# Kernel optimization log

Measured on AMD Instinct MI355X. Metric: run time of the kernel, lower is better.

Reference implementation:

```python
import jax, jax.numpy as jnp
import numpy as np

_IDENTITY = jnp.array([1, 0, 0, 0], dtype=jnp.float32)

G, T, P, B = 512, 128, 256, 512  # num_graphs, max_terms, n_params, batch


def setup_inputs() -> dict:
    key = jax.random.key(0)
    k0, k1, k2, k3, k4 = jax.random.split(key, 5)
    psi_const = jax.random.randint(k0, (G, T), 0, 2).astype(jnp.int32)
    psi_params = jax.random.randint(k1, (G, T, P), 0, 2).astype(jnp.float32)
    phi_const = jax.random.randint(k2, (G, T), 0, 2).astype(jnp.int32)
    phi_params = jax.random.randint(k3, (G, T, P), 0, 2).astype(jnp.float32)
    param_vals = jax.random.randint(k4, (B, P), 0, 2).astype(jnp.float32)
    return {
        "psi_const": psi_const,
        "psi_params": psi_params,
        "phi_const": phi_const,
        "phi_params": phi_params,
        "param_vals": param_vals,
    }


def reference(psi_const, psi_params, phi_const, phi_params, param_vals):
    # GF(2) matmul: contract bitmasks with binary parameter values, mod 2.
    # psi_params: (G,T,P), param_vals: (B,P) -> (B,G,T)
    psi = jnp.mod(psi_const[None].astype(jnp.float32)
                  + jnp.einsum("gtp,bp->bgt", psi_params, param_vals), 2.0)
    phi = jnp.mod(phi_const[None].astype(jnp.float32)
                  + jnp.einsum("gtp,bp->bgt", phi_params, param_vals), 2.0)
    # Elementwise parity product and mod-2 sum over terms -> (B,G)
    exponent = jnp.mod(psi * phi, 2.0)
    sum_exponents = jnp.mod(jnp.sum(exponent, axis=-1), 2.0)
    # Parity-to-sign: (-1)^e = 1 - 2e, embedded as exact scalar (B,G,4)
    summands_exact = (1.0 - 2.0 * sum_exponents)[..., None] * _IDENTITY
    return summands_exact
```

## Files before the change

### kernel.cpp

```cpp
#include <hip/hip_runtime.h>

typedef unsigned long long u64;

#define G 512
#define T 128
#define P 256
#define B 512

struct __align__(16) U64x2 { u64 x, y; };

__global__ __launch_bounds__(256) void pack_pv_kernel(
    const float* __restrict__ pv, u64* __restrict__ out)
{
    int lane = threadIdx.x & 63;
    int wave = threadIdx.x >> 6;
    int row  = blockIdx.x * 4 + wave;
    const float4* src = (const float4*)(pv + (size_t)row * P);
    float4 f = src[lane];
    u64 w0 = __ballot(f.x != 0.0f);
    u64 w1 = __ballot(f.y != 0.0f);
    u64 w2 = __ballot(f.z != 0.0f);
    u64 w3 = __ballot(f.w != 0.0f);
    if (lane == 0) {
        out[row * 4 + 0] = w0;
        out[row * 4 + 1] = w1;
        out[row * 4 + 2] = w2;
        out[row * 4 + 3] = w3;
    }
}

__global__ __launch_bounds__(512) void pi_main_kernel(
    const int*   __restrict__ psi_const,
    const float* __restrict__ psi_params,
    const int*   __restrict__ phi_const,
    const float* __restrict__ phi_params,
    const u64*   __restrict__ pv,
    float4*      __restrict__ out)
{
    __shared__ __align__(16) u64 rows[T * 8];
    __shared__ unsigned code_sm[T];

    const int g    = blockIdx.x;
    const int tid  = threadIdx.x;
    const int lane = tid & 63;
    const int wave = tid >> 6;

    if (tid < T) {
        unsigned pc = ((unsigned)psi_const[g * T + tid]) & 1u;
        unsigned qc = ((unsigned)phi_const[g * T + tid]) & 1u;
        code_sm[tid] = pc | (qc << 1);
    }

    for (int i = 0; i < 32; ++i) {
        int r = wave * 32 + i;
        int t = r & (T - 1);
        const float* mat = (r < T) ? psi_params : phi_params;
        int off = (r < T) ? 0 : 4;
        const float4* src = (const float4*)(mat + ((size_t)g * T + t) * P);
        float4 f = src[lane];
        u64 w0 = __ballot(f.x != 0.0f);
        u64 w1 = __ballot(f.y != 0.0f);
        u64 w2 = __ballot(f.z != 0.0f);
        u64 w3 = __ballot(f.w != 0.0f);
        if (lane == 0) {
            U64x2* d = (U64x2*)&rows[t * 8 + off];
            U64x2 a; a.x = w0; a.y = w1;
            U64x2 c; c.x = w2; c.y = w3;
            d[0] = a;
            d[1] = c;
        }
    }
    __syncthreads();

    const int b = tid;
    const u64* v = pv + (size_t)b * 4;
    u64 v0 = v[0], v1 = v[1], v2 = v[2], v3 = v[3];

    unsigned e = 0;
    #pragma unroll 8
    for (int t = 0; t < T; ++t) {
        const U64x2* row = (const U64x2*)&rows[t * 8];
        U64x2 p0 = row[0], p1 = row[1], q0 = row[2], q1 = row[3];
        u64 ma = (p0.x & v0) ^ (p0.y & v1) ^ (p1.x & v2) ^ (p1.y & v3);
        u64 mb = (q0.x & v0) ^ (q0.y & v1) ^ (q1.x & v2) ^ (q1.y & v3);
        unsigned c = code_sm[t];
        e ^= (((unsigned)__popcll(ma) ^ c) & ((unsigned)__popcll(mb) ^ (c >> 1)));
    }
    e &= 1u;

    float s = 1.0f - 2.0f * (float)e;
    out[(size_t)b * G + g] = make_float4(s, 0.0f, 0.0f, 0.0f);
}

extern "C" void kernel_launch(void* const* d_in, const int* in_sizes, int n_in,
                              void* d_out, int out_size, void* d_ws, size_t ws_size,
                              hipStream_t stream) {
    const int*   psi_const  = (const int*)  d_in[0];
    const float* psi_params = (const float*)d_in[1];
    const int*   phi_const  = (const int*)  d_in[2];
    const float* phi_params = (const float*)d_in[3];
    const float* param_vals = (const float*)d_in[4];

    u64* pv_packed = (u64*)d_ws;

    pack_pv_kernel<<<B / 4, 256, 0, stream>>>(param_vals, pv_packed);
    pi_main_kernel<<<G, 512, 0, stream>>>(psi_const, psi_params,
                                          phi_const, phi_params,
                                          pv_packed, (float4*)d_out);
}
```

Baseline: 182.2 us.

## Split matrix bit-packing into a separate grid-wide kernel and read packed rows from global

Bit-packing of the psi/phi parameter matrices moves out of the main kernel into a standalone kernel over 2048 blocks, and the const vectors are packed into bitmasks by another kernel. The main kernel then runs 1024 blocks of 256 threads, each streaming the packed rows from global memory (broadcast across the wave) instead of from shared memory. The goal is more parallelism on the bandwidth-bound 128 MB float read, which was previously done by only 512 blocks that then had to wait at a barrier. In exchange it adds two kernel launches, a workspace round trip for the packed rows, and uniform global loads inside the inner loop.

New measurement: 196.2 us. +7.7%, slower.

```diff
diff --git a/kernel.cpp b/kernel.cpp
--- a/kernel.cpp
+++ b/kernel.cpp
@@ -22,69 +22,90 @@
     u64 w2 = __ballot(f.z != 0.0f);
     u64 w3 = __ballot(f.w != 0.0f);
     if (lane == 0) {
-        out[row * 4 + 0] = w0;
-        out[row * 4 + 1] = w1;
-        out[row * 4 + 2] = w2;
-        out[row * 4 + 3] = w3;
+        U64x2* d = (U64x2*)(out + row * 4);
+        U64x2 a; a.x = w0; a.y = w1;
+        U64x2 c; c.x = w2; c.y = w3;
+        d[0] = a;
+        d[1] = c;
     }
 }
 
-__global__ __launch_bounds__(512) void pi_main_kernel(
-    const int*   __restrict__ psi_const,
-    const float* __restrict__ psi_params,
-    const int*   __restrict__ phi_const,
-    const float* __restrict__ phi_params,
-    const u64*   __restrict__ pv,
-    float4*      __restrict__ out)
+__global__ __launch_bounds__(256) void pack_codes_kernel(
+    const int* __restrict__ psi_c, const int* __restrict__ phi_c,
+    u64* __restrict__ codes)
 {
-    __shared__ __align__(16) u64 rows[T * 8];
-    __shared__ unsigned code_sm[T];
+    int lane = threadIdx.x & 63;
+    int wave = threadIdx.x >> 6;
+    int g = blockIdx.x * 4 + wave;
+    u64 a0 = __ballot(psi_c[g * T + lane]      != 0);
+    u64 a1 = __ballot(psi_c[g * T + 64 + lane] != 0);
+    u64 b0 = __ballot(phi_c[g * T + lane]      != 0);
+    u64 b1 = __ballot(phi_c[g * T + 64 + lane] != 0);
+    if (lane == 0) {
+        U64x2* d = (U64x2*)(codes + g * 4);
+        U64x2 x; x.x = a0; x.y = a1;
+        U64x2 y; y.x = b0; y.y = b1;
+        d[0] = x;
+        d[1] = y;
+    }
+}
 
-    const int g    = blockIdx.x;
-    const int tid  = threadIdx.x;
-    const int lane = tid & 63;
-    const int wave = tid >> 6;
-
-    if (tid < T) {
-        unsigned pc = ((unsigned)psi_const[g * T + tid]) & 1u;
-        unsigned qc = ((unsigned)phi_const[g * T + tid]) & 1u;
-        code_sm[tid] = pc | (qc << 1);
-    }
-
-    for (int i = 0; i < 32; ++i) {
-        int r = wave * 32 + i;
-        int t = r & (T - 1);
-        const float* mat = (r < T) ? psi_params : phi_params;
-        int off = (r < T) ? 0 : 4;
-        const float4* src = (const float4*)(mat + ((size_t)g * T + t) * P);
+__global__ __launch_bounds__(256) void pack_mat_kernel(
+    const float* __restrict__ psi, const float* __restrict__ phi,
+    u64* __restrict__ rows)
+{
+    int lane = threadIdx.x & 63;
+    int wave = threadIdx.x >> 6;
+    int wid  = blockIdx.x * 4 + wave;
+    #pragma unroll 4
+    for (int j = 0; j < 16; ++j) {
+        int item = wid * 16 + j;
+        int m = item >> 16;
+        int r = item & 65535;
+        const float* mat = m ? phi : psi;
+        const float4* src = (const float4*)(mat + (size_t)r * P);
         float4 f = src[lane];
         u64 w0 = __ballot(f.x != 0.0f);
         u64 w1 = __ballot(f.y != 0.0f);
         u64 w2 = __ballot(f.z != 0.0f);
         u64 w3 = __ballot(f.w != 0.0f);
         if (lane == 0) {
-            U64x2* d = (U64x2*)&rows[t * 8 + off];
+            U64x2* d = (U64x2*)(rows + (size_t)r * 8 + m * 4);
             U64x2 a; a.x = w0; a.y = w1;
             U64x2 c; c.x = w2; c.y = w3;
             d[0] = a;
             d[1] = c;
         }
     }
-    __syncthreads();
+}
 
-    const int b = tid;
+__global__ __launch_bounds__(256) void pi_main_kernel(
+    const u64* __restrict__ rows,
+    const u64* __restrict__ codes,
+    const u64* __restrict__ pv,
+    float4*    __restrict__ out)
+{
+    const int g = blockIdx.x >> 1;
+    const int b = ((blockIdx.x & 1) << 8) | threadIdx.x;
+
     const u64* v = pv + (size_t)b * 4;
     u64 v0 = v[0], v1 = v[1], v2 = v[2], v3 = v[3];
 
+    const u64* rp = rows + (size_t)g * (T * 8);
+
     unsigned e = 0;
-    #pragma unroll 8
-    for (int t = 0; t < T; ++t) {
-        const U64x2* row = (const U64x2*)&rows[t * 8];
-        U64x2 p0 = row[0], p1 = row[1], q0 = row[2], q1 = row[3];
-        u64 ma = (p0.x & v0) ^ (p0.y & v1) ^ (p1.x & v2) ^ (p1.y & v3);
-        u64 mb = (q0.x & v0) ^ (q0.y & v1) ^ (q1.x & v2) ^ (q1.y & v3);
-        unsigned c = code_sm[t];
-        e ^= (((unsigned)__popcll(ma) ^ c) & ((unsigned)__popcll(mb) ^ (c >> 1)));
+    for (int blk = 0; blk < 2; ++blk) {
+        u64 pcw = codes[g * 4 + blk];
+        u64 qcw = codes[g * 4 + 2 + blk];
+        const u64* r = rp + blk * 64 * 8;
+        #pragma unroll 4
+        for (int i = 0; i < 64; ++i, r += 8) {
+            u64 ma = (r[0] & v0) ^ (r[1] & v1) ^ (r[2] & v2) ^ (r[3] & v3);
+            u64 mb = (r[4] & v0) ^ (r[5] & v1) ^ (r[6] & v2) ^ (r[7] & v3);
+            unsigned pa = (unsigned)__popcll(ma) ^ (unsigned)(pcw >> i);
+            unsigned pb = (unsigned)__popcll(mb) ^ (unsigned)(qcw >> i);
+            e ^= pa & pb;
+        }
     }
     e &= 1u;
 
@@ -101,10 +122,13 @@
     const float* phi_params = (const float*)d_in[3];
     const float* param_vals = (const float*)d_in[4];
 
-    u64* pv_packed = (u64*)d_ws;
+    u64* ws    = (u64*)d_ws;
+    u64* rows  = ws;
+    u64* codes = ws + (size_t)G * T * 8;
+    u64* pv    = codes + (size_t)G * 4;
 
-    pack_pv_kernel<<<B / 4, 256, 0, stream>>>(param_vals, pv_packed);
-    pi_main_kernel<<<G, 512, 0, stream>>>(psi_const, psi_params,
-                                          phi_const, phi_params,
-                                          pv_packed, (float4*)d_out);
+    pack_pv_kernel   <<<B / 4, 256, 0, stream>>>(param_vals, pv);
+    pack_codes_kernel<<<G / 4, 256, 0, stream>>>(psi_const, phi_const, codes);
+    pack_mat_kernel  <<<2048,  256, 0, stream>>>(psi_params, phi_params, rows);
+    pi_main_kernel   <<<G * 2, 256, 0, stream>>>(rows, codes, pv, (float4*)d_out);
 }
```
